# Kernel optimization log

Measured on AMD Instinct MI355X. Metric: run time of the kernel, lower is better.

Reference implementation:

```python
import jax, jax.numpy as jnp
import numpy as np

B, T, N, F = 32, 36, 10000, 3
HORIZON = 10
NUM_REGIONS = 20
NAN_RATE = 0.05


def setup_inputs() -> dict:
    key = jax.random.key(0)
    k1, k2, k3 = jax.random.split(key, 3)
    seq = jax.random.normal(k1, (B, T, N, F), dtype=jnp.float32)
    nan_mask = jax.random.uniform(k2, (B, T, N, F)) < NAN_RATE
    seq = jnp.where(nan_mask, jnp.nan, seq)
    cluster_id = jax.random.randint(k3, (N,), 0, NUM_REGIONS, dtype=jnp.int64)
    return {"seq": seq, "cluster_id": cluster_id}


def _nanmean_all(x):
    valid = ~jnp.isnan(x)
    s = jnp.where(valid, x, 0.0).sum()
    c = valid.sum().astype(x.dtype)
    return s / c


def reference(seq, cluster_id):
    x = seq[..., 0]                               # [B, T, N] speed channel
    valid = ~jnp.isnan(x)
    xz = jnp.where(valid, x, 0.0)
    cnt = valid.sum(axis=1).astype(x.dtype)       # [B, N]
    time_mean = xz.sum(axis=1) / cnt              # [B, N]; NaN if a node is all-NaN
    pred_speed = jnp.tile(time_mean[:, None, :], (1, HORIZON, 1))  # [B, 10, N]

    # per-region nanmean over nodes: segment-mean via one-hot contraction
    onehot = (cluster_id[:, None] == jnp.arange(NUM_REGIONS)).astype(x.dtype)  # [N, R]
    pvalid = ~jnp.isnan(pred_speed)
    pz = jnp.where(pvalid, pred_speed, 0.0)
    rsum = jnp.einsum('bhn,nr->bhr', pz, onehot)                     # [B, 10, R]
    rcnt = jnp.einsum('bhn,nr->bhr', pvalid.astype(x.dtype), onehot)  # [B, 10, R]
    regional = rsum / rcnt                                            # NaN if region all-NaN

    # nan_to_global_avg: replace remaining NaNs with global nanmean of each tensor
    g1 = _nanmean_all(pred_speed)
    g2 = _nanmean_all(regional)
    out_pred = jnp.where(jnp.isnan(pred_speed), g1, pred_speed)
    out_regional = jnp.where(jnp.isnan(regional), g2, regional)
    return out_pred, out_regional
```

## Files before the change

### kernel.cpp

```cpp
#include <hip/hip_runtime.h>

#define BB 32
#define TT 36
#define NN 10000
#define FF 3
#define HH 10
#define RR 20
#define NQ (NN / 4)
#define NC (NN * FF / 4)


__global__ __launch_bounds__(256) void k_time_mean(
        const float4* __restrict__ seq4,
        const int* __restrict__ cid,
        float* __restrict__ tm,
        float* __restrict__ rsum,
        float* __restrict__ rcnt) {
    __shared__ float ls[RR];
    __shared__ float lc[RR];
    const int b = blockIdx.y;
    const int c = blockIdx.x * blockDim.x + threadIdx.x;
    if (threadIdx.x < RR) { ls[threadIdx.x] = 0.f; lc[threadIdx.x] = 0.f; }
    __syncthreads();

    if (c < NC) {
        const int k = c / 3;
        const int r = c - 3 * k;
        const float4* p = seq4 + (size_t)b * TT * NC + c;

        float sA = 0.f, sB = 0.f;
        int   cA = 0,   cB = 0;
        #pragma unroll
        for (int t = 0; t < TT; ++t) {
            const float4 a = p[(size_t)t * NC];
            const float vA = (r == 0) ? a.x : ((r == 1) ? a.z : a.y);
            const float vB = a.w;
            if (vA == vA)           { sA += vA; cA++; }
            if (r == 0 && vB == vB) { sB += vB; cB++; }
        }

        const float nanf_ = __int_as_float(0x7fc00000);
        const int nA = (r == 0) ? 4 * k : ((r == 1) ? 4 * k + 2 : 4 * k + 3);
        const float mA = cA ? sA / (float)cA : nanf_;
        tm[b * NN + nA] = mA;
        if (cA) {
            const int rg = cid[nA];
            atomicAdd(&ls[rg], mA);
            atomicAdd(&lc[rg], 1.f);
        }
        if (r == 0) {
            const int nB = 4 * k + 1;
            const float mB = cB ? sB / (float)cB : nanf_;
            tm[b * NN + nB] = mB;
            if (cB) {
                const int rg = cid[nB];
                atomicAdd(&ls[rg], mB);
                atomicAdd(&lc[rg], 1.f);
            }
        }
    }

    __syncthreads();
    if (threadIdx.x < RR) {
        atomicAdd(&rsum[b * RR + threadIdx.x], ls[threadIdx.x]);
        atomicAdd(&rcnt[b * RR + threadIdx.x], lc[threadIdx.x]);
    }
}

__global__ void k_regional(const float* __restrict__ rsum,
                           const float* __restrict__ rcnt,
                           float* __restrict__ g1out,
                           float* __restrict__ out_reg) {
    const int tid = threadIdx.x;
    __shared__ float sv[10], sc[10], ss[10], sn[10];
    __shared__ float g2s;

    float myrs = 0.f, myrc = 0.f;
    float val = 0.f;
    int valid = 0;
    if (tid < BB * RR) {
        myrs = rsum[tid];
        myrc = rcnt[tid];
        if (myrc > 0.f) { val = myrs / myrc; valid = 1; }
    }

    float wv = valid ? val : 0.f;
    float wc = (float)valid;
    float ws = myrs;
    float wn = myrc;
    for (int off = 32; off > 0; off >>= 1) {
        wv += __shfl_down(wv, off, 64);
        wc += __shfl_down(wc, off, 64);
        ws += __shfl_down(ws, off, 64);
        wn += __shfl_down(wn, off, 64);
    }
    const int wave = tid >> 6;
    if ((tid & 63) == 0) { sv[wave] = wv; sc[wave] = wc; ss[wave] = ws; sn[wave] = wn; }
    __syncthreads();

    if (tid == 0) {
        float v = 0.f, cc = 0.f, s = 0.f, n = 0.f;
        #pragma unroll
        for (int i = 0; i < 10; ++i) { v += sv[i]; cc += sc[i]; s += ss[i]; n += sn[i]; }
        g2s = v / cc;
        g1out[0] = s / n;
    }
    __syncthreads();

    if (tid < BB * RR) {
        const int b = tid / RR, r = tid % RR;
        const float o = valid ? val : g2s;
        #pragma unroll
        for (int h = 0; h < HH; ++h)
            out_reg[(size_t)(b * HH + h) * RR + r] = o;
    }
}

__global__ __launch_bounds__(256) void k_pred(
        const float* __restrict__ tm,
        const float* __restrict__ g1p,
        float* __restrict__ out) {
    const int b = blockIdx.y;
    const int q = blockIdx.x * blockDim.x + threadIdx.x;
    if (q >= NQ) return;
    const float g1 = g1p[0];
    float4 v = ((const float4*)tm)[(size_t)b * NQ + q];
    if (!(v.x == v.x)) v.x = g1;
    if (!(v.y == v.y)) v.y = g1;
    if (!(v.z == v.z)) v.z = g1;
    if (!(v.w == v.w)) v.w = g1;
    float4* o = (float4*)out + (size_t)b * HH * NQ + q;
    #pragma unroll
    for (int h = 0; h < HH; ++h)
        o[(size_t)h * NQ] = v;
}

extern "C" void kernel_launch(void* const* d_in, const int* in_sizes, int n_in,
                              void* d_out, int out_size, void* d_ws, size_t ws_size,
                              hipStream_t stream) {
    const float* seq = (const float*)d_in[0];
    const int*   cid = (const int*)d_in[1];
    float* out = (float*)d_out;

    float* ws   = (float*)d_ws;
    float* tm   = ws;
    float* rsum = tm + BB * NN;
    float* rcnt = rsum + BB * RR;
    float* g1   = rcnt + BB * RR;

    hipMemsetAsync(rsum, 0, (size_t)(2 * BB * RR) * sizeof(float), stream);

    dim3 blk(256);
    dim3 grdA((NC + 255) / 256, BB);
    dim3 grdP((NQ + 255) / 256, BB);
    k_time_mean<<<grdA, blk, 0, stream>>>((const float4*)seq, cid, tm, rsum, rcnt);
    k_regional<<<1, 640, 0, stream>>>(rsum, rcnt, g1,
                                      out + (size_t)BB * HH * NN);
    k_pred<<<grdP, blk, 0, stream>>>(tm, g1, out);
}
```

Before: 209.0 us.

## Replace global atomics with per-block partials and fuse regional and pred kernels

The time-mean kernel now writes per-block regional partial sums and counts instead of atomically accumulating into global buffers, which removes the memset launch. The separate regional and pred kernels are merged into one launch: one extra block computes the regional outputs, and each pred block reduces all partials to g1 only when its tile contains a NaN. This saves two launches and a serial single-block dependency, at the cost of redundant global reductions in blocks that hit NaNs.

Result: no change. 207.3 us (-0.8%).

```diff
diff --git a/kernel.cpp b/kernel.cpp
--- a/kernel.cpp
+++ b/kernel.cpp
@@ -8,14 +8,16 @@
 #define RR 20
 #define NQ (NN / 4)
 #define NC (NN * FF / 4)
+#define NPB ((NC + 255) / 256)
+#define PB ((NQ + 255) / 256)
 
 
 __global__ __launch_bounds__(256) void k_time_mean(
         const float4* __restrict__ seq4,
         const int* __restrict__ cid,
         float* __restrict__ tm,
-        float* __restrict__ rsum,
-        float* __restrict__ rcnt) {
+        float* __restrict__ psum,
+        float* __restrict__ pcnt) {
     __shared__ float ls[RR];
     __shared__ float lc[RR];
     const int b = blockIdx.y;
@@ -62,77 +64,95 @@
 
     __syncthreads();
     if (threadIdx.x < RR) {
-        atomicAdd(&rsum[b * RR + threadIdx.x], ls[threadIdx.x]);
-        atomicAdd(&rcnt[b * RR + threadIdx.x], lc[threadIdx.x]);
+        const int o = (b * NPB + blockIdx.x) * RR + threadIdx.x;
+        psum[o] = ls[threadIdx.x];
+        pcnt[o] = lc[threadIdx.x];
     }
 }
 
-__global__ void k_regional(const float* __restrict__ rsum,
-                           const float* __restrict__ rcnt,
-                           float* __restrict__ g1out,
-                           float* __restrict__ out_reg) {
+__global__ __launch_bounds__(256) void k_fused(
+        const float* __restrict__ tm,
+        const float* __restrict__ psum,
+        const float* __restrict__ pcnt,
+        float* __restrict__ out) {
     const int tid = threadIdx.x;
-    __shared__ float sv[10], sc[10], ss[10], sn[10];
-    __shared__ float g2s;
+    const int gb = blockIdx.x;
+    __shared__ float shs[4], shc[4];
 
-    float myrs = 0.f, myrc = 0.f;
-    float val = 0.f;
-    int valid = 0;
-    if (tid < BB * RR) {
-        myrs = rsum[tid];
-        myrc = rcnt[tid];
-        if (myrc > 0.f) { val = myrs / myrc; valid = 1; }
+    if (gb < BB * PB) {
+        const int b = gb / PB;
+        const int q = (gb - b * PB) * 256 + tid;
+        float4 v = {0.f, 0.f, 0.f, 0.f};
+        int bad = 0;
+        if (q < NQ) {
+            v = ((const float4*)tm)[(size_t)b * NQ + q];
+            bad = (!(v.x == v.x)) | (!(v.y == v.y)) |
+                  (!(v.z == v.z)) | (!(v.w == v.w));
+        }
+        if (__syncthreads_or(bad)) {
+            float s = 0.f, cc = 0.f;
+            for (int i = tid; i < BB * NPB * RR; i += 256) {
+                s += psum[i]; cc += pcnt[i];
+            }
+            for (int off = 32; off > 0; off >>= 1) {
+                s  += __shfl_down(s,  off, 64);
+                cc += __shfl_down(cc, off, 64);
+            }
+            if ((tid & 63) == 0) { shs[tid >> 6] = s; shc[tid >> 6] = cc; }
+            __syncthreads();
+            const float g1 = (shs[0] + shs[1] + shs[2] + shs[3]) /
+                             (shc[0] + shc[1] + shc[2] + shc[3]);
+            if (!(v.x == v.x)) v.x = g1;
+            if (!(v.y == v.y)) v.y = g1;
+            if (!(v.z == v.z)) v.z = g1;
+            if (!(v.w == v.w)) v.w = g1;
+        }
+        if (q < NQ) {
+            float4* o = (float4*)out + (size_t)b * HH * NQ + q;
+            #pragma unroll
+            for (int h = 0; h < HH; ++h)
+                o[(size_t)h * NQ] = v;
+        }
+    } else {
+        float val[3]; int vd[3];
+        float sv = 0.f, sc = 0.f;
+        #pragma unroll
+        for (int j = 0; j < 3; ++j) {
+            val[j] = 0.f; vd[j] = 0;
+            const int i = tid + j * 256;
+            if (i < BB * RR) {
+                const int b = i / RR, r = i - b * RR;
+                float s = 0.f, c = 0.f;
+                #pragma unroll
+                for (int x = 0; x < NPB; ++x) {
+                    const int o = (b * NPB + x) * RR + r;
+                    s += psum[o];
+                    c += pcnt[o];
+                }
+                if (c > 0.f) { val[j] = s / c; vd[j] = 1; sv += val[j]; sc += 1.f; }
+            }
+        }
+        for (int off = 32; off > 0; off >>= 1) {
+            sv += __shfl_down(sv, off, 64);
+            sc += __shfl_down(sc, off, 64);
+        }
+        if ((tid & 63) == 0) { shs[tid >> 6] = sv; shc[tid >> 6] = sc; }
+        __syncthreads();
+        const float g2 = (shs[0] + shs[1] + shs[2] + shs[3]) /
+                         (shc[0] + shc[1] + shc[2] + shc[3]);
+        float* out_reg = out + (size_t)BB * HH * NN;
+        #pragma unroll
+        for (int j = 0; j < 3; ++j) {
+            const int i = tid + j * 256;
+            if (i < BB * RR) {
+                const int b = i / RR, r = i - b * RR;
+                const float o = vd[j] ? val[j] : g2;
+                #pragma unroll
+                for (int h = 0; h < HH; ++h)
+                    out_reg[(size_t)(b * HH + h) * RR + r] = o;
+            }
+        }
     }
-
-    float wv = valid ? val : 0.f;
-    float wc = (float)valid;
-    float ws = myrs;
-    float wn = myrc;
-    for (int off = 32; off > 0; off >>= 1) {
-        wv += __shfl_down(wv, off, 64);
-        wc += __shfl_down(wc, off, 64);
-        ws += __shfl_down(ws, off, 64);
-        wn += __shfl_down(wn, off, 64);
-    }
-    const int wave = tid >> 6;
-    if ((tid & 63) == 0) { sv[wave] = wv; sc[wave] = wc; ss[wave] = ws; sn[wave] = wn; }
-    __syncthreads();
-
-    if (tid == 0) {
-        float v = 0.f, cc = 0.f, s = 0.f, n = 0.f;
-        #pragma unroll
-        for (int i = 0; i < 10; ++i) { v += sv[i]; cc += sc[i]; s += ss[i]; n += sn[i]; }
-        g2s = v / cc;
-        g1out[0] = s / n;
-    }
-    __syncthreads();
-
-    if (tid < BB * RR) {
-        const int b = tid / RR, r = tid % RR;
-        const float o = valid ? val : g2s;
-        #pragma unroll
-        for (int h = 0; h < HH; ++h)
-            out_reg[(size_t)(b * HH + h) * RR + r] = o;
-    }
-}
-
-__global__ __launch_bounds__(256) void k_pred(
-        const float* __restrict__ tm,
-        const float* __restrict__ g1p,
-        float* __restrict__ out) {
-    const int b = blockIdx.y;
-    const int q = blockIdx.x * blockDim.x + threadIdx.x;
-    if (q >= NQ) return;
-    const float g1 = g1p[0];
-    float4 v = ((const float4*)tm)[(size_t)b * NQ + q];
-    if (!(v.x == v.x)) v.x = g1;
-    if (!(v.y == v.y)) v.y = g1;
-    if (!(v.z == v.z)) v.z = g1;
-    if (!(v.w == v.w)) v.w = g1;
-    float4* o = (float4*)out + (size_t)b * HH * NQ + q;
-    #pragma unroll
-    for (int h = 0; h < HH; ++h)
-        o[(size_t)h * NQ] = v;
 }
 
 extern "C" void kernel_launch(void* const* d_in, const int* in_sizes, int n_in,
@@ -144,17 +164,11 @@
 
     float* ws   = (float*)d_ws;
     float* tm   = ws;
-    float* rsum = tm + BB * NN;
-    float* rcnt = rsum + BB * RR;
-    float* g1   = rcnt + BB * RR;
-
-    hipMemsetAsync(rsum, 0, (size_t)(2 * BB * RR) * sizeof(float), stream);
+    float* psum = tm + BB * NN;
+    float* pcnt = psum + BB * NPB * RR;
 
     dim3 blk(256);
-    dim3 grdA((NC + 255) / 256, BB);
-    dim3 grdP((NQ + 255) / 256, BB);
-    k_time_mean<<<grdA, blk, 0, stream>>>((const float4*)seq, cid, tm, rsum, rcnt);
-    k_regional<<<1, 640, 0, stream>>>(rsum, rcnt, g1,
-                                      out + (size_t)BB * HH * NN);
-    k_pred<<<grdP, blk, 0, stream>>>(tm, g1, out);
+    dim3 grdA(NPB, BB);
+    k_time_mean<<<grdA, blk, 0, stream>>>((const float4*)seq, cid, tm, psum, pcnt);
+    k_fused<<<dim3(BB * PB + 1), blk, 0, stream>>>(tm, psum, pcnt, out);
 }
```
